# Optimization experiments

Measured on AMD Instinct MI355X. Metric: run time of the kernel, lower is better.

## Reference

```python
import jax, jax.numpy as jnp
import numpy as np

B, N = 2, 65536
V, VSUB, J, R = 6890, 689, 24, 64
THRESH = 0.12


def trilinear(grid, coords):
    # grid: [C, D, H, W]; coords: [..., 3] in [-1, 1] (x->W, y->H, z->D)
    C, D, H, W = grid.shape
    cs = jnp.clip(coords.reshape(-1, 3), -1.0, 1.0)
    x = (cs[:, 0] + 1.0) * 0.5 * (W - 1)
    y = (cs[:, 1] + 1.0) * 0.5 * (H - 1)
    z = (cs[:, 2] + 1.0) * 0.5 * (D - 1)
    x0 = jnp.floor(x).astype(jnp.int32); x1 = jnp.minimum(x0 + 1, W - 1)
    y0 = jnp.floor(y).astype(jnp.int32); y1 = jnp.minimum(y0 + 1, H - 1)
    z0 = jnp.floor(z).astype(jnp.int32); z1 = jnp.minimum(z0 + 1, D - 1)
    fx = x - x0; fy = y - y0; fz = z - z0
    g = lambda zi, yi, xi: grid[:, zi, yi, xi]  # [C, M]
    out = (g(z0, y0, x0) * ((1 - fz) * (1 - fy) * (1 - fx))
         + g(z0, y0, x1) * ((1 - fz) * (1 - fy) * fx)
         + g(z0, y1, x0) * ((1 - fz) * fy * (1 - fx))
         + g(z0, y1, x1) * ((1 - fz) * fy * fx)
         + g(z1, y0, x0) * (fz * (1 - fy) * (1 - fx))
         + g(z1, y0, x1) * (fz * (1 - fy) * fx)
         + g(z1, y1, x0) * (fz * fy * (1 - fx))
         + g(z1, y1, x1) * (fz * fy * fx))
    return out.T.reshape(coords.shape[:-1] + (C,))


def setup_inputs() -> dict:
    key = jax.random.key(0)
    ks = jax.random.split(key, 8)
    pts_in = jax.random.normal(ks[0], (B, N, 3), jnp.float32) * 0.4
    vs_template = jax.random.normal(ks[1], (1, VSUB, 3), jnp.float32) * 0.4
    shape_offset = jax.random.normal(ks[2], (1, V, 3), jnp.float32) * 0.01
    init_idx = jax.random.randint(ks[3], (N, 3), 0, V, jnp.int32)
    bar = jax.random.uniform(ks[4], (N, 3), jnp.float32) + 1e-3
    init_bar = bar / jnp.sum(bar, -1, keepdims=True)
    lbs_voxel = jax.nn.softmax(jax.random.normal(ks[5], (J, R, R, R), jnp.float32), axis=0)
    tfs = jnp.tile(jnp.eye(4, dtype=jnp.float32), (B, J, 1, 1)) \
        + 0.05 * jax.random.normal(ks[6], (B, J, 4, 4), jnp.float32)
    grid_scale = jnp.full((3,), 1.5, jnp.float32)
    grid_offset = jnp.zeros((3,), jnp.float32)
    return dict(pts_in=pts_in, vs_template=vs_template, shape_offset=shape_offset,
                init_idx=init_idx, init_bar=init_bar, lbs_voxel=lbs_voxel,
                tfs=tfs, grid_scale=grid_scale, grid_offset=grid_offset)


def reference(pts_in, vs_template, shape_offset, init_idx, init_bar, lbs_voxel, tfs, grid_scale, grid_offset):
    # --- KNN (K=1) against subsampled template vertices ---
    v = vs_template[0]  # [VSUB, 3]
    d2 = (jnp.sum(pts_in * pts_in, -1, keepdims=True)
          + jnp.sum(v * v, -1)[None, None, :]
          - 2.0 * jnp.einsum('bnd,vd->bnv', pts_in, v))  # [B,N,VSUB]
    dist_sq = jnp.min(d2, axis=-1)  # [B,N]
    mask = (dist_sq < THRESH ** 2)[..., None]  # [B,N,1]
    # --- barycentric interpolation of per-vertex shape offsets ---
    tri = shape_offset[0][init_idx]               # [N,3,3]
    off = jnp.sum(init_bar[..., None] * tri, -2)  # [N,3]
    pts = pts_in + off[None]
    # --- query LBS weights from explicit voxel grid (fast-SNARF) ---
    pts_norm = (pts - grid_offset) * grid_scale
    w = trilinear(lbs_voxel, pts_norm)  # [B,N,J]
    w = w / jnp.clip(jnp.sum(w, -1, keepdims=True), 1e-6, None)
    # --- forward skinning ---
    w_tf = jnp.einsum('bnj,bjkl->bnkl', w, tfs)  # [B,N,4,4]
    pts_h = jnp.concatenate([pts, jnp.ones_like(pts[..., :1])], -1)  # [B,N,4]
    pts_posed = jnp.einsum('bnkl,bnl->bnk', w_tf, pts_h)[..., :3]
    pts_cano_all = pts_posed.reshape(B, N, 1, 3)
    return pts_cano_all, mask, w_tf
```

## Files before the change

kernel.cpp:

```cpp
#include <hip/hip_runtime.h>
#include <math.h>

#define NB    2
#define NPTS  65536
#define NVSUB 689
#define NJ    24
#define GR    64
#define GRV   (GR*GR*GR)
#define THRESH2 0.0144f

#define O_PTS  0
#define O_MASK (NB*NPTS*3)
#define O_WTF  (O_MASK + NB*NPTS)

#define WS_VS4_OFF (GRV * NJ)

__global__ __launch_bounds__(256) void prep_kernel(const float* __restrict__ g,
                                                   const float* __restrict__ vs,
                                                   float* __restrict__ ws) {
    if (blockIdx.x < GRV / 256) {
        int vox = blockIdx.x * 256 + threadIdx.x;
        float v[NJ];
#pragma unroll
        for (int c = 0; c < NJ; ++c) v[c] = g[c * GRV + vox];
        float4* dst = (float4*)(ws + (size_t)vox * NJ);
#pragma unroll
        for (int c4 = 0; c4 < 6; ++c4)
            dst[c4] = make_float4(v[4*c4+0], v[4*c4+1], v[4*c4+2], v[4*c4+3]);
    } else {
        float4* vs4 = (float4*)(ws + WS_VS4_OFF);
        for (int i = threadIdx.x; i < NVSUB; i += 256) {
            float x = vs[i * 3 + 0], y = vs[i * 3 + 1], z = vs[i * 3 + 2];
            vs4[i] = make_float4(x, y, z, x * x + y * y + z * z);
        }
    }
}

__global__ __launch_bounds__(256, 4) void snarf_main(
    const float* __restrict__ pts_in,
    const float* __restrict__ shape_off,
    const int*   __restrict__ init_idx,
    const float* __restrict__ init_bar,
    const float* __restrict__ ws,
    const float* __restrict__ tfs,
    const float* __restrict__ gscale,
    const float* __restrict__ goff,
    float* __restrict__ out) {
    __shared__ float s_m[NB][4][64];
    __shared__ float s_part[NB][64][20];

    const int tid  = threadIdx.x;
    const int q    = tid >> 6;
    const int nl   = tid & 63;
    const int b    = q & 1;
    const int half = q >> 1;
    const int n    = blockIdx.x * 64 + nl;

    const float4* vs4 = (const float4*)(ws + WS_VS4_OFF);
    const float*  gT  = ws;

    const float p0x = pts_in[n * 3 + 0], p0y = pts_in[n * 3 + 1], p0z = pts_in[n * 3 + 2];
    const float p1x = pts_in[(NPTS + n) * 3 + 0], p1y = pts_in[(NPTS + n) * 3 + 1],
                p1z = pts_in[(NPTS + n) * 3 + 2];

    const int vbeg = q * 172 + (q != 0);
    const int vend = (q + 1) * 172 + 1;
    float m0a = 3.4e38f, m0b = 3.4e38f, m1a = 3.4e38f, m1b = 3.4e38f;
    int v = vbeg;
    for (; v + 4 <= vend; v += 4) {
        float4 t0 = vs4[v], t1 = vs4[v + 1], t2 = vs4[v + 2], t3 = vs4[v + 3];
        m0a = fminf(m0a, fmaf(-2.f, p0x * t0.x + p0y * t0.y + p0z * t0.z, t0.w));
        m1a = fminf(m1a, fmaf(-2.f, p1x * t0.x + p1y * t0.y + p1z * t0.z, t0.w));
        m0b = fminf(m0b, fmaf(-2.f, p0x * t1.x + p0y * t1.y + p0z * t1.z, t1.w));
        m1b = fminf(m1b, fmaf(-2.f, p1x * t1.x + p1y * t1.y + p1z * t1.z, t1.w));
        m0a = fminf(m0a, fmaf(-2.f, p0x * t2.x + p0y * t2.y + p0z * t2.z, t2.w));
        m1a = fminf(m1a, fmaf(-2.f, p1x * t2.x + p1y * t2.y + p1z * t2.z, t2.w));
        m0b = fminf(m0b, fmaf(-2.f, p0x * t3.x + p0y * t3.y + p0z * t3.z, t3.w));
        m1b = fminf(m1b, fmaf(-2.f, p1x * t3.x + p1y * t3.y + p1z * t3.z, t3.w));
    }
    for (; v < vend; ++v) {
        float4 t0 = vs4[v];
        m0a = fminf(m0a, fmaf(-2.f, p0x * t0.x + p0y * t0.y + p0z * t0.z, t0.w));
        m1a = fminf(m1a, fmaf(-2.f, p1x * t0.x + p1y * t0.y + p1z * t0.z, t0.w));
    }
    s_m[0][q][nl] = fminf(m0a, m0b);
    s_m[1][q][nl] = fminf(m1a, m1b);
    __syncthreads();

    int i0 = init_idx[n * 3 + 0] * 3;
    int i1 = init_idx[n * 3 + 1] * 3;
    int i2 = init_idx[n * 3 + 2] * 3;
    float b0 = init_bar[n * 3 + 0], b1 = init_bar[n * 3 + 1], b2 = init_bar[n * 3 + 2];
    float ox = b0 * shape_off[i0 + 0] + b1 * shape_off[i1 + 0] + b2 * shape_off[i2 + 0];
    float oy = b0 * shape_off[i0 + 1] + b1 * shape_off[i1 + 1] + b2 * shape_off[i2 + 1];
    float oz = b0 * shape_off[i0 + 2] + b1 * shape_off[i1 + 2] + b2 * shape_off[i2 + 2];

    const float qx = (b ? p1x : p0x) + ox;
    const float qy = (b ? p1y : p0y) + oy;
    const float qz = (b ? p1z : p0z) + oz;

    float cx = fminf(fmaxf((qx - goff[0]) * gscale[0], -1.f), 1.f);
    float cy = fminf(fmaxf((qy - goff[1]) * gscale[1], -1.f), 1.f);
    float cz = fminf(fmaxf((qz - goff[2]) * gscale[2], -1.f), 1.f);
    float x = (cx + 1.f) * 0.5f * (GR - 1);
    float y = (cy + 1.f) * 0.5f * (GR - 1);
    float z = (cz + 1.f) * 0.5f * (GR - 1);
    int x0 = (int)floorf(x), y0 = (int)floorf(y), z0 = (int)floorf(z);
    int x1 = min(x0 + 1, GR - 1), y1 = min(y0 + 1, GR - 1), z1 = min(z0 + 1, GR - 1);
    float fx = x - (float)x0, fy = y - (float)y0, fz = z - (float)z0;
    float wx[2] = {1.f - fx, fx}, wy[2] = {1.f - fy, fy}, wz[2] = {1.f - fz, fz};

    const int jbeg = half * 12;
    float w[12];
#pragma unroll
    for (int c = 0; c < 12; ++c) w[c] = 0.f;

#pragma unroll
    for (int ci = 0; ci < 8; ++ci) {
        int xi = (ci & 1) ? x1 : x0;
        int yi = (ci & 2) ? y1 : y0;
        int zi = (ci & 4) ? z1 : z0;
        float wt = wx[ci & 1] * wy[(ci >> 1) & 1] * wz[(ci >> 2) & 1];
        int vox = (zi * GR + yi) * GR + xi;
        const float4* g4 = (const float4*)(gT + (size_t)vox * NJ + jbeg);
        float4 g0 = g4[0], g1 = g4[1], g2 = g4[2];
        w[0]  = fmaf(wt, g0.x, w[0]);  w[1]  = fmaf(wt, g0.y, w[1]);
        w[2]  = fmaf(wt, g0.z, w[2]);  w[3]  = fmaf(wt, g0.w, w[3]);
        w[4]  = fmaf(wt, g1.x, w[4]);  w[5]  = fmaf(wt, g1.y, w[5]);
        w[6]  = fmaf(wt, g1.z, w[6]);  w[7]  = fmaf(wt, g1.w, w[7]);
        w[8]  = fmaf(wt, g2.x, w[8]);  w[9]  = fmaf(wt, g2.y, w[9]);
        w[10] = fmaf(wt, g2.z, w[10]); w[11] = fmaf(wt, g2.w, w[11]);
    }
    float wsum = 0.f;
#pragma unroll
    for (int c = 0; c < 12; ++c) wsum += w[c];

    const int bu = __builtin_amdgcn_readfirstlane(b);
    const int jbu = __builtin_amdgcn_readfirstlane(jbeg);
    const float* tb = tfs + (size_t)(bu * NJ + jbu) * 16;
    float acc[16];
#pragma unroll
    for (int k = 0; k < 16; ++k) acc[k] = 0.f;
#pragma unroll
    for (int jj = 0; jj < 12; ++jj) {
        float wj = w[jj];
#pragma unroll
        for (int k = 0; k < 16; ++k) acc[k] = fmaf(wj, tb[jj * 16 + k], acc[k]);
    }

    if (half == 1) {
        float* sp = &s_part[b][nl][0];
        ((float4*)sp)[0] = make_float4(acc[0],  acc[1],  acc[2],  acc[3]);
        ((float4*)sp)[1] = make_float4(acc[4],  acc[5],  acc[6],  acc[7]);
        ((float4*)sp)[2] = make_float4(acc[8],  acc[9],  acc[10], acc[11]);
        ((float4*)sp)[3] = make_float4(acc[12], acc[13], acc[14], acc[15]);
        sp[16] = wsum;
    }
    __syncthreads();

    if (half == 0) {
        const float* sp = &s_part[b][nl][0];
        float4 q0 = ((const float4*)sp)[0], q1 = ((const float4*)sp)[1];
        float4 q2 = ((const float4*)sp)[2], q3 = ((const float4*)sp)[3];
        acc[0] += q0.x;  acc[1] += q0.y;  acc[2] += q0.z;  acc[3] += q0.w;
        acc[4] += q1.x;  acc[5] += q1.y;  acc[6] += q1.z;  acc[7] += q1.w;
        acc[8] += q2.x;  acc[9] += q2.y;  acc[10] += q2.z; acc[11] += q2.w;
        acc[12] += q3.x; acc[13] += q3.y; acc[14] += q3.z; acc[15] += q3.w;
        wsum += sp[16];
        float inv = __builtin_amdgcn_rcpf(fmaxf(wsum, 1e-6f));
#pragma unroll
        for (int k = 0; k < 16; ++k) acc[k] *= inv;

        float px = acc[0] * qx + acc[1] * qy + acc[2]  * qz + acc[3];
        float py = acc[4] * qx + acc[5] * qy + acc[6]  * qz + acc[7];
        float pz = acc[8] * qx + acc[9] * qy + acc[10] * qz + acc[11];

        float mm = fminf(fminf(s_m[b][0][nl], s_m[b][1][nl]),
                         fminf(s_m[b][2][nl], s_m[b][3][nl]));
        float pbx = b ? p1x : p0x, pby = b ? p1y : p0y, pbz = b ? p1z : p0z;
        float dist2 = mm + pbx * pbx + pby * pby + pbz * pbz;

        size_t bn = (size_t)b * NPTS + n;
        out[O_PTS + bn * 3 + 0] = px;
        out[O_PTS + bn * 3 + 1] = py;
        out[O_PTS + bn * 3 + 2] = pz;
        out[O_MASK + bn] = (dist2 < THRESH2) ? 1.f : 0.f;
        float4* wt4 = (float4*)(out + O_WTF + bn * 16);
        wt4[0] = make_float4(acc[0],  acc[1],  acc[2],  acc[3]);
        wt4[1] = make_float4(acc[4],  acc[5],  acc[6],  acc[7]);
        wt4[2] = make_float4(acc[8],  acc[9],  acc[10], acc[11]);
        wt4[3] = make_float4(acc[12], acc[13], acc[14], acc[15]);
    }
}

__global__ __launch_bounds__(256) void snarf_fallback(
    const float* __restrict__ pts_in, const float* __restrict__ vs,
    const float* __restrict__ shape_off, const int* __restrict__ init_idx,
    const float* __restrict__ init_bar, const float* __restrict__ grid,
    const float* __restrict__ tfs, const float* __restrict__ gscale,
    const float* __restrict__ goff, float* __restrict__ out) {
    const int n = blockIdx.x * 256 + threadIdx.x;
    for (int b = 0; b < NB; ++b) {
        float px = pts_in[((size_t)b * NPTS + n) * 3 + 0];
        float py = pts_in[((size_t)b * NPTS + n) * 3 + 1];
        float pz = pts_in[((size_t)b * NPTS + n) * 3 + 2];
        float mm = 3.4e38f;
        for (int v = 0; v < NVSUB; ++v) {
            float dx = px - vs[v * 3 + 0], dy = py - vs[v * 3 + 1], dz = pz - vs[v * 3 + 2];
            mm = fminf(mm, dx * dx + dy * dy + dz * dz);
        }
        int i0 = init_idx[n * 3 + 0] * 3, i1 = init_idx[n * 3 + 1] * 3, i2 = init_idx[n * 3 + 2] * 3;
        float b0 = init_bar[n * 3 + 0], b1 = init_bar[n * 3 + 1], b2 = init_bar[n * 3 + 2];
        float qx = px + b0 * shape_off[i0 + 0] + b1 * shape_off[i1 + 0] + b2 * shape_off[i2 + 0];
        float qy = py + b0 * shape_off[i0 + 1] + b1 * shape_off[i1 + 1] + b2 * shape_off[i2 + 1];
        float qz = pz + b0 * shape_off[i0 + 2] + b1 * shape_off[i1 + 2] + b2 * shape_off[i2 + 2];
        float cx = fminf(fmaxf((qx - goff[0]) * gscale[0], -1.f), 1.f);
        float cy = fminf(fmaxf((qy - goff[1]) * gscale[1], -1.f), 1.f);
        float cz = fminf(fmaxf((qz - goff[2]) * gscale[2], -1.f), 1.f);
        float x = (cx + 1.f) * 0.5f * (GR - 1), y = (cy + 1.f) * 0.5f * (GR - 1), z = (cz + 1.f) * 0.5f * (GR - 1);
        int x0 = (int)floorf(x), y0 = (int)floorf(y), z0 = (int)floorf(z);
        int x1 = min(x0 + 1, GR - 1), y1 = min(y0 + 1, GR - 1), z1 = min(z0 + 1, GR - 1);
        float fx = x - x0, fy = y - y0, fz = z - z0;
        float wxa[2] = {1.f - fx, fx}, wya[2] = {1.f - fy, fy}, wza[2] = {1.f - fz, fz};
        float w[NJ];
        for (int c = 0; c < NJ; ++c) w[c] = 0.f;
        for (int ci = 0; ci < 8; ++ci) {
            int xi = (ci & 1) ? x1 : x0, yi = (ci & 2) ? y1 : y0, zi = (ci & 4) ? z1 : z0;
            float wt = wxa[ci & 1] * wya[(ci >> 1) & 1] * wza[(ci >> 2) & 1];
            int vox = (zi * GR + yi) * GR + xi;
            for (int c = 0; c < NJ; ++c) w[c] = fmaf(wt, grid[c * GRV + vox], w[c]);
        }
        float s = 0.f;
        for (int c = 0; c < NJ; ++c) s += w[c];
        float inv = 1.f / fmaxf(s, 1e-6f);
        float acc[16];
        for (int k = 0; k < 16; ++k) acc[k] = 0.f;
        for (int j = 0; j < NJ; ++j) {
            float wj = w[j] * inv;
            for (int k = 0; k < 16; ++k) acc[k] = fmaf(wj, tfs[(b * NJ + j) * 16 + k], acc[k]);
        }
        size_t bn = (size_t)b * NPTS + n;
        out[O_PTS + bn * 3 + 0] = acc[0] * qx + acc[1] * qy + acc[2] * qz + acc[3];
        out[O_PTS + bn * 3 + 1] = acc[4] * qx + acc[5] * qy + acc[6] * qz + acc[7];
        out[O_PTS + bn * 3 + 2] = acc[8] * qx + acc[9] * qy + acc[10] * qz + acc[11];
        out[O_MASK + bn] = (mm < THRESH2) ? 1.f : 0.f;
        for (int k = 0; k < 16; ++k) out[O_WTF + bn * 16 + k] = acc[k];
    }
}

extern "C" void kernel_launch(void* const* d_in, const int* in_sizes, int n_in,
                              void* d_out, int out_size, void* d_ws, size_t ws_size,
                              hipStream_t stream) {
    const float* pts_in    = (const float*)d_in[0];
    const float* vs        = (const float*)d_in[1];
    const float* shape_off = (const float*)d_in[2];
    const int*   init_idx  = (const int*)d_in[3];
    const float* init_bar  = (const float*)d_in[4];
    const float* lbs       = (const float*)d_in[5];
    const float* tfs       = (const float*)d_in[6];
    const float* gs        = (const float*)d_in[7];
    const float* go        = (const float*)d_in[8];
    float* out = (float*)d_out;

    const size_t needed = ((size_t)GRV * NJ + NVSUB * 4) * sizeof(float);
    if (ws_size >= needed) {
        float* wsf = (float*)d_ws;
        prep_kernel<<<GRV / 256 + 1, 256, 0, stream>>>(lbs, vs, wsf);
        snarf_main<<<NPTS / 64, 256, 0, stream>>>(
            pts_in, shape_off, init_idx, init_bar, wsf, tfs, gs, go, out);
    } else {
        snarf_fallback<<<NPTS / 256, 256, 0, stream>>>(
            pts_in, vs, shape_off, init_idx, init_bar, lbs, tfs, gs, go, out);
    }
}
```

Before: 146.2 us.

## Split KNN mask into its own kernel with LDS-staged template vertices

Moves the nearest-vertex distance computation out of the fused kernel into a separate mask kernel. In that kernel each point is split across 4 lanes, the template vertices are staged in shared memory, and the lanes combine results with shuffles. The deform kernel now maps one point per lane pair (128 points per block, 2 halves over joints), drops the KNN work, and loses one block-wide sync. The cost is an extra kernel launch, re-reading points in both kernels, and each mask block rebuilding the vertex table in LDS.

```diff
diff --git a/kernel.cpp b/kernel.cpp
--- a/kernel.cpp
+++ b/kernel.cpp
@@ -13,104 +13,102 @@
 #define O_MASK (NB*NPTS*3)
 #define O_WTF  (O_MASK + NB*NPTS)
 
-#define WS_VS4_OFF (GRV * NJ)
-
 __global__ __launch_bounds__(256) void prep_kernel(const float* __restrict__ g,
+                                                   float* __restrict__ gt) {
+    int vox = blockIdx.x * 256 + threadIdx.x;
+    float v[NJ];
+#pragma unroll
+    for (int c = 0; c < NJ; ++c) v[c] = g[c * GRV + vox];
+    float4* dst = (float4*)(gt + (size_t)vox * NJ);
+#pragma unroll
+    for (int c4 = 0; c4 < 6; ++c4)
+        dst[c4] = make_float4(v[4*c4+0], v[4*c4+1], v[4*c4+2], v[4*c4+3]);
+}
+
+__global__ __launch_bounds__(256) void mask_kernel(const float* __restrict__ pts_in,
                                                    const float* __restrict__ vs,
-                                                   float* __restrict__ ws) {
-    if (blockIdx.x < GRV / 256) {
-        int vox = blockIdx.x * 256 + threadIdx.x;
-        float v[NJ];
-#pragma unroll
-        for (int c = 0; c < NJ; ++c) v[c] = g[c * GRV + vox];
-        float4* dst = (float4*)(ws + (size_t)vox * NJ);
-#pragma unroll
-        for (int c4 = 0; c4 < 6; ++c4)
-            dst[c4] = make_float4(v[4*c4+0], v[4*c4+1], v[4*c4+2], v[4*c4+3]);
-    } else {
-        float4* vs4 = (float4*)(ws + WS_VS4_OFF);
-        for (int i = threadIdx.x; i < NVSUB; i += 256) {
-            float x = vs[i * 3 + 0], y = vs[i * 3 + 1], z = vs[i * 3 + 2];
-            vs4[i] = make_float4(x, y, z, x * x + y * y + z * z);
-        }
-    }
-}
-
-__global__ __launch_bounds__(256, 4) void snarf_main(
+                                                   float* __restrict__ out) {
+    __shared__ float4 s_vs[NVSUB];
+    const int tid = threadIdx.x;
+    for (int i = tid; i < NVSUB; i += 256) {
+        float x = vs[i * 3 + 0], y = vs[i * 3 + 1], z = vs[i * 3 + 2];
+        s_vs[i] = make_float4(x, y, z, x * x + y * y + z * z);
+    }
+    __syncthreads();
+
+    const int t  = blockIdx.x * 256 + tid;
+    const int p  = t >> 2;
+    const int qq = t & 3;
+    const int b  = p >> 16;
+    const int n  = p & (NPTS - 1);
+
+    const float* P = pts_in + ((size_t)b * NPTS + n) * 3;
+    const float px = P[0], py = P[1], pz = P[2];
+
+    const int vbeg = qq * 173;
+    const int vend = min(vbeg + 173, NVSUB);
+    float ma = 3.4e38f, mb = 3.4e38f;
+    int v = vbeg;
+    for (; v + 2 <= vend; v += 2) {
+        float4 t0 = s_vs[v];
+        float4 t1 = s_vs[v + 1];
+        ma = fminf(ma, fmaf(-2.f, px * t0.x + py * t0.y + pz * t0.z, t0.w));
+        mb = fminf(mb, fmaf(-2.f, px * t1.x + py * t1.y + pz * t1.z, t1.w));
+    }
+    if (v < vend) {
+        float4 t0 = s_vs[v];
+        ma = fminf(ma, fmaf(-2.f, px * t0.x + py * t0.y + pz * t0.z, t0.w));
+    }
+    float mm = fminf(ma, mb);
+    mm = fminf(mm, __shfl_xor(mm, 1));
+    mm = fminf(mm, __shfl_xor(mm, 2));
+    if (qq == 0) {
+        float dist2 = mm + px * px + py * py + pz * pz;
+        out[O_MASK + p] = (dist2 < THRESH2) ? 1.f : 0.f;
+    }
+}
+
+__global__ __launch_bounds__(256) void deform_kernel(
     const float* __restrict__ pts_in,
     const float* __restrict__ shape_off,
     const int*   __restrict__ init_idx,
     const float* __restrict__ init_bar,
-    const float* __restrict__ ws,
+    const float* __restrict__ gT,
     const float* __restrict__ tfs,
     const float* __restrict__ gscale,
     const float* __restrict__ goff,
     float* __restrict__ out) {
-    __shared__ float s_m[NB][4][64];
-    __shared__ float s_part[NB][64][20];
-
-    const int tid  = threadIdx.x;
-    const int q    = tid >> 6;
-    const int nl   = tid & 63;
-    const int b    = q & 1;
-    const int half = q >> 1;
-    const int n    = blockIdx.x * 64 + nl;
-
-    const float4* vs4 = (const float4*)(ws + WS_VS4_OFF);
-    const float*  gT  = ws;
-
-    const float p0x = pts_in[n * 3 + 0], p0y = pts_in[n * 3 + 1], p0z = pts_in[n * 3 + 2];
-    const float p1x = pts_in[(NPTS + n) * 3 + 0], p1y = pts_in[(NPTS + n) * 3 + 1],
-                p1z = pts_in[(NPTS + n) * 3 + 2];
-
-    const int vbeg = q * 172 + (q != 0);
-    const int vend = (q + 1) * 172 + 1;
-    float m0a = 3.4e38f, m0b = 3.4e38f, m1a = 3.4e38f, m1b = 3.4e38f;
-    int v = vbeg;
-    for (; v + 4 <= vend; v += 4) {
-        float4 t0 = vs4[v], t1 = vs4[v + 1], t2 = vs4[v + 2], t3 = vs4[v + 3];
-        m0a = fminf(m0a, fmaf(-2.f, p0x * t0.x + p0y * t0.y + p0z * t0.z, t0.w));
-        m1a = fminf(m1a, fmaf(-2.f, p1x * t0.x + p1y * t0.y + p1z * t0.z, t0.w));
-        m0b = fminf(m0b, fmaf(-2.f, p0x * t1.x + p0y * t1.y + p0z * t1.z, t1.w));
-        m1b = fminf(m1b, fmaf(-2.f, p1x * t1.x + p1y * t1.y + p1z * t1.z, t1.w));
-        m0a = fminf(m0a, fmaf(-2.f, p0x * t2.x + p0y * t2.y + p0z * t2.z, t2.w));
-        m1a = fminf(m1a, fmaf(-2.f, p1x * t2.x + p1y * t2.y + p1z * t2.z, t2.w));
-        m0b = fminf(m0b, fmaf(-2.f, p0x * t3.x + p0y * t3.y + p0z * t3.z, t3.w));
-        m1b = fminf(m1b, fmaf(-2.f, p1x * t3.x + p1y * t3.y + p1z * t3.z, t3.w));
-    }
-    for (; v < vend; ++v) {
-        float4 t0 = vs4[v];
-        m0a = fminf(m0a, fmaf(-2.f, p0x * t0.x + p0y * t0.y + p0z * t0.z, t0.w));
-        m1a = fminf(m1a, fmaf(-2.f, p1x * t0.x + p1y * t0.y + p1z * t0.z, t0.w));
-    }
-    s_m[0][q][nl] = fminf(m0a, m0b);
-    s_m[1][q][nl] = fminf(m1a, m1b);
-    __syncthreads();
+    __shared__ float s_part[128][20];
+
+    const int tid = threadIdx.x;
+    const int pl  = tid & 127;
+    const int hf  = tid >> 7;
+    const int p   = blockIdx.x * 128 + pl;
+    const int b   = p >> 16;
+    const int n   = p & (NPTS - 1);
+
+    const float* P = pts_in + ((size_t)b * NPTS + n) * 3;
+    const float px = P[0], py = P[1], pz = P[2];
 
     int i0 = init_idx[n * 3 + 0] * 3;
     int i1 = init_idx[n * 3 + 1] * 3;
     int i2 = init_idx[n * 3 + 2] * 3;
     float b0 = init_bar[n * 3 + 0], b1 = init_bar[n * 3 + 1], b2 = init_bar[n * 3 + 2];
-    float ox = b0 * shape_off[i0 + 0] + b1 * shape_off[i1 + 0] + b2 * shape_off[i2 + 0];
-    float oy = b0 * shape_off[i0 + 1] + b1 * shape_off[i1 + 1] + b2 * shape_off[i2 + 1];
-    float oz = b0 * shape_off[i0 + 2] + b1 * shape_off[i1 + 2] + b2 * shape_off[i2 + 2];
-
-    const float qx = (b ? p1x : p0x) + ox;
-    const float qy = (b ? p1y : p0y) + oy;
-    const float qz = (b ? p1z : p0z) + oz;
-
-    float cx = fminf(fmaxf((qx - goff[0]) * gscale[0], -1.f), 1.f);
-    float cy = fminf(fmaxf((qy - goff[1]) * gscale[1], -1.f), 1.f);
-    float cz = fminf(fmaxf((qz - goff[2]) * gscale[2], -1.f), 1.f);
-    float x = (cx + 1.f) * 0.5f * (GR - 1);
-    float y = (cy + 1.f) * 0.5f * (GR - 1);
-    float z = (cz + 1.f) * 0.5f * (GR - 1);
+    float qx = px + b0 * shape_off[i0 + 0] + b1 * shape_off[i1 + 0] + b2 * shape_off[i2 + 0];
+    float qy = py + b0 * shape_off[i0 + 1] + b1 * shape_off[i1 + 1] + b2 * shape_off[i2 + 1];
+    float qz = pz + b0 * shape_off[i0 + 2] + b1 * shape_off[i1 + 2] + b2 * shape_off[i2 + 2];
+
+    float ccx = fminf(fmaxf((qx - goff[0]) * gscale[0], -1.f), 1.f);
+    float ccy = fminf(fmaxf((qy - goff[1]) * gscale[1], -1.f), 1.f);
+    float ccz = fminf(fmaxf((qz - goff[2]) * gscale[2], -1.f), 1.f);
+    float x = (ccx + 1.f) * 0.5f * (GR - 1);
+    float y = (ccy + 1.f) * 0.5f * (GR - 1);
+    float z = (ccz + 1.f) * 0.5f * (GR - 1);
     int x0 = (int)floorf(x), y0 = (int)floorf(y), z0 = (int)floorf(z);
     int x1 = min(x0 + 1, GR - 1), y1 = min(y0 + 1, GR - 1), z1 = min(z0 + 1, GR - 1);
     float fx = x - (float)x0, fy = y - (float)y0, fz = z - (float)z0;
-    float wx[2] = {1.f - fx, fx}, wy[2] = {1.f - fy, fy}, wz[2] = {1.f - fz, fz};
-
-    const int jbeg = half * 12;
+    float wxa[2] = {1.f - fx, fx}, wya[2] = {1.f - fy, fy}, wza[2] = {1.f - fz, fz};
+
     float w[12];
 #pragma unroll
     for (int c = 0; c < 12; ++c) w[c] = 0.f;
@@ -120,9 +118,9 @@
         int xi = (ci & 1) ? x1 : x0;
         int yi = (ci & 2) ? y1 : y0;
         int zi = (ci & 4) ? z1 : z0;
-        float wt = wx[ci & 1] * wy[(ci >> 1) & 1] * wz[(ci >> 2) & 1];
+        float wt = wxa[ci & 1] * wya[(ci >> 1) & 1] * wza[(ci >> 2) & 1];
         int vox = (zi * GR + yi) * GR + xi;
-        const float4* g4 = (const float4*)(gT + (size_t)vox * NJ + jbeg);
+        const float4* g4 = (const float4*)(gT + (size_t)vox * NJ + hf * 12);
         float4 g0 = g4[0], g1 = g4[1], g2 = g4[2];
         w[0]  = fmaf(wt, g0.x, w[0]);  w[1]  = fmaf(wt, g0.y, w[1]);
         w[2]  = fmaf(wt, g0.z, w[2]);  w[3]  = fmaf(wt, g0.w, w[3]);
@@ -135,9 +133,9 @@
 #pragma unroll
     for (int c = 0; c < 12; ++c) wsum += w[c];
 
-    const int bu = __builtin_amdgcn_readfirstlane(b);
-    const int jbu = __builtin_amdgcn_readfirstlane(jbeg);
-    const float* tb = tfs + (size_t)(bu * NJ + jbu) * 16;
+    const int bu  = __builtin_amdgcn_readfirstlane(b);
+    const int hfu = __builtin_amdgcn_readfirstlane(hf);
+    const float* tb = tfs + (size_t)(bu * NJ + hfu * 12) * 16;
     float acc[16];
 #pragma unroll
     for (int k = 0; k < 16; ++k) acc[k] = 0.f;
@@ -148,8 +146,8 @@
         for (int k = 0; k < 16; ++k) acc[k] = fmaf(wj, tb[jj * 16 + k], acc[k]);
     }
 
-    if (half == 1) {
-        float* sp = &s_part[b][nl][0];
+    if (hf == 1) {
+        float* sp = &s_part[pl][0];
         ((float4*)sp)[0] = make_float4(acc[0],  acc[1],  acc[2],  acc[3]);
         ((float4*)sp)[1] = make_float4(acc[4],  acc[5],  acc[6],  acc[7]);
         ((float4*)sp)[2] = make_float4(acc[8],  acc[9],  acc[10], acc[11]);
@@ -158,8 +156,8 @@
     }
     __syncthreads();
 
-    if (half == 0) {
-        const float* sp = &s_part[b][nl][0];
+    if (hf == 0) {
+        const float* sp = &s_part[pl][0];
         float4 q0 = ((const float4*)sp)[0], q1 = ((const float4*)sp)[1];
         float4 q2 = ((const float4*)sp)[2], q3 = ((const float4*)sp)[3];
         acc[0] += q0.x;  acc[1] += q0.y;  acc[2] += q0.z;  acc[3] += q0.w;
@@ -171,20 +169,14 @@
 #pragma unroll
         for (int k = 0; k < 16; ++k) acc[k] *= inv;
 
-        float px = acc[0] * qx + acc[1] * qy + acc[2]  * qz + acc[3];
-        float py = acc[4] * qx + acc[5] * qy + acc[6]  * qz + acc[7];
-        float pz = acc[8] * qx + acc[9] * qy + acc[10] * qz + acc[11];
-
-        float mm = fminf(fminf(s_m[b][0][nl], s_m[b][1][nl]),
-                         fminf(s_m[b][2][nl], s_m[b][3][nl]));
-        float pbx = b ? p1x : p0x, pby = b ? p1y : p0y, pbz = b ? p1z : p0z;
-        float dist2 = mm + pbx * pbx + pby * pby + pbz * pbz;
-
-        size_t bn = (size_t)b * NPTS + n;
-        out[O_PTS + bn * 3 + 0] = px;
-        out[O_PTS + bn * 3 + 1] = py;
-        out[O_PTS + bn * 3 + 2] = pz;
-        out[O_MASK + bn] = (dist2 < THRESH2) ? 1.f : 0.f;
+        float ox = acc[0] * qx + acc[1] * qy + acc[2]  * qz + acc[3];
+        float oy = acc[4] * qx + acc[5] * qy + acc[6]  * qz + acc[7];
+        float oz = acc[8] * qx + acc[9] * qy + acc[10] * qz + acc[11];
+
+        size_t bn = (size_t)p;
+        out[O_PTS + bn * 3 + 0] = ox;
+        out[O_PTS + bn * 3 + 1] = oy;
+        out[O_PTS + bn * 3 + 2] = oz;
         float4* wt4 = (float4*)(out + O_WTF + bn * 16);
         wt4[0] = make_float4(acc[0],  acc[1],  acc[2],  acc[3]);
         wt4[1] = make_float4(acc[4],  acc[5],  acc[6],  acc[7]);
@@ -262,12 +254,13 @@
     const float* go        = (const float*)d_in[8];
     float* out = (float*)d_out;
 
-    const size_t needed = ((size_t)GRV * NJ + NVSUB * 4) * sizeof(float);
+    const size_t needed = (size_t)GRV * NJ * sizeof(float);
     if (ws_size >= needed) {
-        float* wsf = (float*)d_ws;
-        prep_kernel<<<GRV / 256 + 1, 256, 0, stream>>>(lbs, vs, wsf);
-        snarf_main<<<NPTS / 64, 256, 0, stream>>>(
-            pts_in, shape_off, init_idx, init_bar, wsf, tfs, gs, go, out);
+        float* gT = (float*)d_ws;
+        prep_kernel<<<GRV / 256, 256, 0, stream>>>(lbs, gT);
+        mask_kernel<<<(NB * NPTS * 4) / 256, 256, 0, stream>>>(pts_in, vs, out);
+        deform_kernel<<<(NB * NPTS) / 128, 256, 0, stream>>>(
+            pts_in, shape_off, init_idx, init_bar, gT, tfs, gs, go, out);
     } else {
         snarf_fallback<<<NPTS / 256, 256, 0, stream>>>(
             pts_in, vs, shape_off, init_idx, init_bar, lbs, tfs, gs, go, out);
```

New measurement: 151.0 us. 3.2% more time.
